# Optimization experiments

Measured on AMD Instinct MI355X. Metric: run time of the kernel, lower is better.

Reference implementation:

```python
import jax, jax.numpy as jnp
import numpy as np

S, B, D, H = 2048, 4, 1024, 16
HD = D // H  # 64
NEG = -1e9


def _rope_cache(seq_len, dim, base=10000.0):
    inv_freq = 1.0 / (base ** (jnp.arange(0, dim, 2, dtype=jnp.float32) / dim))
    pos = jnp.arange(seq_len, dtype=jnp.float32)
    freqs = jnp.einsum('i,j->ij', pos, inv_freq)          # [S, dim/2]
    emb = jnp.concatenate([freqs, freqs], axis=-1)         # [S, dim]
    return jnp.cos(emb)[None, None], jnp.sin(emb)[None, None]  # [1,1,S,dim]


def _apply_rotary(x, cos, sin):
    # rotated[..., ::2] = -x[..., 1::2]; rotated[..., 1::2] = x[..., ::2]
    x_even = x[..., ::2]
    x_odd = x[..., 1::2]
    rotated = jnp.stack([-x_odd, x_even], axis=-1).reshape(x.shape)
    return x * cos + rotated * sin


def setup_inputs() -> dict:
    key = jax.random.key(0)
    kx, kq, ko = jax.random.split(key, 3)
    x = jax.random.normal(kx, (S, B, D), dtype=jnp.float32)
    # additive causal mask, broadcastable over [B,H,S,S]
    causal = jnp.triu(jnp.full((S, S), NEG, dtype=jnp.float32), k=1)
    cos, sin = _rope_cache(S, HD)
    Wqkv = jax.random.normal(kq, (D, 3 * D), dtype=jnp.float32) * (D ** -0.5)
    Wout = jax.random.normal(ko, (D, D), dtype=jnp.float32) * (D ** -0.5)
    return {"x": x, "attn_mask": causal, "cos": cos, "sin": sin,
            "Wqkv": Wqkv, "Wout": Wout}


def reference(x, attn_mask, cos, sin, Wqkv, Wout):
    scale = 1.0 / jnp.sqrt(jnp.float32(HD))
    xb = jnp.swapaxes(x, 0, 1)                       # [B,S,D]
    qkv = jnp.einsum('bsd,de->bse', xb, Wqkv)        # [B,S,3D]
    q, k, v = jnp.split(qkv, 3, axis=-1)
    def heads(t):
        return t.reshape(B, S, H, HD).transpose(0, 2, 1, 3)  # [B,H,S,HD]
    q, k, v = heads(q), heads(k), heads(v)
    q = _apply_rotary(q, cos, sin)
    k = _apply_rotary(k, cos, sin)
    scores = jnp.einsum('bhsd,bhtd->bhst', q, k) * scale + attn_mask
    probs = jax.nn.softmax(scores, axis=-1)
    ctx = jnp.einsum('bhst,bhtd->bhsd', probs, v)
    ctx = ctx.transpose(0, 2, 1, 3).reshape(B, S, D)  # [B,S,D]
    out = jnp.einsum('bsd,de->bse', ctx, Wout)
    return jnp.swapaxes(out, 0, 1)                    # [S,B,D]
```

## Files before the change

kernel.cpp:

```cpp
#include <hip/hip_runtime.h>
#include <hip/hip_bf16.h>

#define S_LEN 2048
#define BATCH 4
#define DMODEL 1024
#define NHEAD 16
#define HDIM 64
#define E3 3072

typedef __bf16 bf16x8 __attribute__((ext_vector_type(8)));
typedef float f32x4 __attribute__((ext_vector_type(4)));

typedef const __attribute__((address_space(1))) void gvoid;
typedef __attribute__((address_space(3))) void lvoid;

__global__ void cast_f32_bf16(const float* __restrict__ src, __bf16* __restrict__ dst) {
    int i = (blockIdx.x * 256 + threadIdx.x) * 8;
    float4 a = *(const float4*)(src + i);
    float4 b = *(const float4*)(src + i + 4);
    bf16x8 v;
    v[0] = (__bf16)a.x; v[1] = (__bf16)a.y; v[2] = (__bf16)a.z; v[3] = (__bf16)a.w;
    v[4] = (__bf16)b.x; v[5] = (__bf16)b.y; v[6] = (__bf16)b.z; v[7] = (__bf16)b.w;
    *(bf16x8*)(dst + i) = v;
}

__global__ void transpose_f32_bf16(const float* __restrict__ src, __bf16* __restrict__ dst,
                                   int R, int C) {
    __shared__ float tile[32][33];
    int c0 = blockIdx.x * 32, r0 = blockIdx.y * 32;
    int tx = threadIdx.x, ty = threadIdx.y;
#pragma unroll
    for (int i = 0; i < 32; i += 8)
        tile[ty + i][tx] = src[(size_t)(r0 + ty + i) * C + c0 + tx];
    __syncthreads();
#pragma unroll
    for (int i = 0; i < 32; i += 8)
        dst[(size_t)(c0 + ty + i) * R + r0 + tx] = (__bf16)tile[tx][ty + i];
}

__global__ void transpose_v(const __bf16* __restrict__ qkv, __bf16* __restrict__ vt) {
    __shared__ unsigned short tile[64][65];
    int bh = blockIdx.y;
    int s0 = blockIdx.x * 64;
    int tx = threadIdx.x & 31, ty = threadIdx.x >> 5;
    const __bf16* src = qkv + (size_t)(bh >> 4) * S_LEN * E3 + 2 * DMODEL + (bh & 15) * HDIM;
#pragma unroll
    for (int i = 0; i < 8; i++) {
        ushort2 v = *(const ushort2*)(src + (size_t)(s0 + ty + i * 8) * E3 + 2 * tx);
        tile[2 * tx][ty + i * 8] = v.x;
        tile[2 * tx + 1][ty + i * 8] = v.y;
    }
    __syncthreads();
    __bf16* dst = vt + (size_t)bh * HDIM * S_LEN + s0;
#pragma unroll
    for (int i = 0; i < 8; i++) {
        ushort2 v;
        v.x = tile[ty + i * 8][2 * tx];
        v.y = tile[ty + i * 8][2 * tx + 1];
        *(ushort2*)(dst + (size_t)(ty + i * 8) * S_LEN + 2 * tx) = v;
    }
}

__global__ __launch_bounds__(256) void gemm_bt(
    const __bf16* __restrict__ A, const __bf16* __restrict__ BT, void* __restrict__ C,
    int K, int aSB, int aSS, int cSB, int cSS, int cF32) {
    __shared__ __bf16 lA[128 * 32];
    __shared__ __bf16 lB[128 * 32];

    const int tid = threadIdx.x;
    const int lane = tid & 63;
    const int quad = lane >> 4, l16 = lane & 15;
    const int wave = tid >> 6;
    const int wm = wave >> 1, wn = wave & 1;
    const int rm0 = blockIdx.y * 128;
    const int n0 = blockIdx.x * 128;
    const int bb = rm0 / S_LEN;
    const int s0 = rm0 % S_LEN;

    const int lrow = lane >> 2;
    const int lch = (lane & 3) * 8;
    const int row0 = wave * 32;
    const __bf16* gA0 = A + (size_t)bb * aSB + (size_t)(s0 + row0 + lrow) * aSS + lch;
    const __bf16* gA1 = A + (size_t)bb * aSB + (size_t)(s0 + row0 + 16 + lrow) * aSS + lch;
    const __bf16* gB0 = BT + (size_t)(n0 + row0 + lrow) * K + lch;
    const __bf16* gB1 = BT + (size_t)(n0 + row0 + 16 + lrow) * K + lch;
    __bf16* ldsA0 = &lA[row0 * 32];
    __bf16* ldsA1 = &lA[(row0 + 16) * 32];
    __bf16* ldsB0 = &lB[row0 * 32];
    __bf16* ldsB1 = &lB[(row0 + 16) * 32];

    f32x4 acc[4][4];
#pragma unroll
    for (int i = 0; i < 4; i++)
#pragma unroll
        for (int j = 0; j < 4; j++) acc[i][j] = (f32x4){0.f, 0.f, 0.f, 0.f};

    for (int k0 = 0; k0 < K; k0 += 32) {
        __builtin_amdgcn_global_load_lds((gvoid*)(gA0 + k0), (lvoid*)ldsA0, 16, 0, 0);
        __builtin_amdgcn_global_load_lds((gvoid*)(gA1 + k0), (lvoid*)ldsA1, 16, 0, 0);
        __builtin_amdgcn_global_load_lds((gvoid*)(gB0 + k0), (lvoid*)ldsB0, 16, 0, 0);
        __builtin_amdgcn_global_load_lds((gvoid*)(gB1 + k0), (lvoid*)ldsB1, 16, 0, 0);
        __syncthreads();

        bf16x8 aF[4], bF[4];
#pragma unroll
        for (int i = 0; i < 4; i++) {
            aF[i] = *(const bf16x8*)&lA[(wm * 64 + i * 16 + l16) * 32 + quad * 8];
            bF[i] = *(const bf16x8*)&lB[(wn * 64 + i * 16 + l16) * 32 + quad * 8];
        }
#pragma unroll
        for (int i = 0; i < 4; i++)
#pragma unroll
            for (int j = 0; j < 4; j++)
                acc[i][j] = __builtin_amdgcn_mfma_f32_16x16x32_bf16(aF[i], bF[j], acc[i][j], 0, 0, 0);
        __syncthreads();
    }

#pragma unroll
    for (int i = 0; i < 4; i++) {
        const int rl = wm * 64 + i * 16 + quad * 4;
#pragma unroll
        for (int r = 0; r < 4; r++) {
            const size_t rowOff = (size_t)bb * cSB + (size_t)(s0 + rl + r) * cSS + n0 + wn * 64 + l16;
            if (cF32) {
                float* cRow = (float*)C + rowOff;
#pragma unroll
                for (int j = 0; j < 4; j++) cRow[j * 16] = acc[i][j][r];
            } else {
                __bf16* cRow = (__bf16*)C + rowOff;
#pragma unroll
                for (int j = 0; j < 4; j++) cRow[j * 16] = (__bf16)acc[i][j][r];
            }
        }
    }
}

__global__ void rope_kernel(__bf16* __restrict__ qkv, const float* __restrict__ cosb,
                            const float* __restrict__ sinb) {
    int idx = blockIdx.x * 256 + threadIdx.x;
    int p2 = (idx & 31) * 2;
    int h = (idx >> 5) & 15;
    int part = (idx >> 9) & 1;
    int row = idx >> 10;
    int s = row & (S_LEN - 1);
    size_t base = (size_t)row * E3 + part * DMODEL + h * HDIM + p2;
    float x0 = (float)qkv[base];
    float x1 = (float)qkv[base + 1];
    float c0 = cosb[s * HDIM + p2];
    float c1 = cosb[s * HDIM + p2 + 1];
    float sn0 = sinb[s * HDIM + p2];
    float sn1 = sinb[s * HDIM + p2 + 1];
    qkv[base] = (__bf16)(x0 * c0 - x1 * sn0);
    qkv[base + 1] = (__bf16)(x1 * c1 + x0 * sn1);
}

#define VT_IDX(hd, t) ((hd) * 72 + ((hd) >> 4) * 8 + (t))

__global__ __launch_bounds__(256) void attn_kernel(const __bf16* __restrict__ qkv,
                                                   const __bf16* __restrict__ vt,
                                                   __bf16* __restrict__ ctx) {
    __shared__ __bf16 sK[64 * 72];
    __shared__ __bf16 sVT[64 * 72 + 32];
    __shared__ __bf16 sP[4 * 2 * 16 * 72];

    const int tid = threadIdx.x, lane = tid & 63, wave = tid >> 6;
    const int quad = lane >> 4, l16 = lane & 15;
    const int b = blockIdx.y >> 4, h = blockIdx.y & 15;
    const int pair = blockIdx.x;
    const int qtA = pair, qtB = 31 - pair;
    const int s0A = qtA * 64 + wave * 16;
    const int s0B = qtB * 64 + wave * 16;
    __bf16* PwA = &sP[wave * 2 * 16 * 72];
    __bf16* PwB = PwA + 16 * 72;

    const int srow = tid >> 2;
    const int c0 = (tid & 3) * 16;

    const float qscale = 0.125f * 1.44269504f;
    const __bf16* kBase = qkv + (size_t)(b * S_LEN + srow) * E3 + DMODEL + h * HDIM + c0;
    const __bf16* vBase = vt + ((size_t)blockIdx.y * HDIM + srow) * S_LEN + c0;

    const __bf16* qbA = qkv + (size_t)(b * S_LEN + s0A) * E3 + h * HDIM + (size_t)l16 * E3;
    const __bf16* qbB = qkv + (size_t)(b * S_LEN + s0B) * E3 + h * HDIM + (size_t)l16 * E3;
    bf16x8 qfA0 = *(const bf16x8*)(qbA + quad * 8);
    bf16x8 qfA1 = *(const bf16x8*)(qbA + 32 + quad * 8);
    bf16x8 qfB0 = *(const bf16x8*)(qbB + quad * 8);
    bf16x8 qfB1 = *(const bf16x8*)(qbB + 32 + quad * 8);
#pragma unroll
    for (int i = 0; i < 8; i++) {
        qfA0[i] = (__bf16)((float)qfA0[i] * qscale);
        qfA1[i] = (__bf16)((float)qfA1[i] * qscale);
        qfB0[i] = (__bf16)((float)qfB0[i] * qscale);
        qfB1[i] = (__bf16)((float)qfB1[i] * qscale);
    }

    f32x4 oA[4], oB[4], lacA, lacB;
#pragma unroll
    for (int j = 0; j < 4; j++) {
        oA[j] = (f32x4){0.f, 0.f, 0.f, 0.f};
        oB[j] = (f32x4){0.f, 0.f, 0.f, 0.f};
    }
    lacA = (f32x4){0.f, 0.f, 0.f, 0.f};
    lacB = (f32x4){0.f, 0.f, 0.f, 0.f};

    bf16x8 ones;
#pragma unroll
    for (int i = 0; i < 8; i++) ones[i] = (__bf16)1.0f;

    const __bf16* kRow = kBase;
    const __bf16* vRow = vBase;
    bf16x8 k0 = *(const bf16x8*)kRow;
    bf16x8 k1 = *(const bf16x8*)(kRow + 8);
    bf16x8 v0 = *(const bf16x8*)vRow;
    bf16x8 v1 = *(const bf16x8*)(vRow + 8);

    const int nT = qtB + 1;
#pragma unroll 1
    for (int it = 0; it < nT; ++it) {
        const int t0 = it * 64;
        *(bf16x8*)&sK[srow * 72 + c0] = k0;
        *(bf16x8*)&sK[srow * 72 + c0 + 8] = k1;
        *(bf16x8*)&sVT[VT_IDX(srow, c0)] = v0;
        *(bf16x8*)&sVT[VT_IDX(srow, c0 + 8)] = v1;
        __syncthreads();

        if (it + 1 < nT) {
            kRow += (size_t)64 * E3;
            vRow += 64;
            k0 = *(const bf16x8*)kRow;
            k1 = *(const bf16x8*)(kRow + 8);
            v0 = *(const bf16x8*)vRow;
            v1 = *(const bf16x8*)(vRow + 8);
        }

        const bool aAct = (it <= qtA);

        f32x4 scA[4], scB[4];
        __builtin_amdgcn_s_setprio(1);
#pragma unroll
        for (int j = 0; j < 4; j++) {
            bf16x8 kf0 = *(const bf16x8*)&sK[(j * 16 + l16) * 72 + quad * 8];
            bf16x8 kf1 = *(const bf16x8*)&sK[(j * 16 + l16) * 72 + 32 + quad * 8];
            f32x4 z = (f32x4){0.f, 0.f, 0.f, 0.f};
            z = __builtin_amdgcn_mfma_f32_16x16x32_bf16(qfB0, kf0, z, 0, 0, 0);
            scB[j] = __builtin_amdgcn_mfma_f32_16x16x32_bf16(qfB1, kf1, z, 0, 0, 0);
            if (aAct) {
                f32x4 za = (f32x4){0.f, 0.f, 0.f, 0.f};
                za = __builtin_amdgcn_mfma_f32_16x16x32_bf16(qfA0, kf0, za, 0, 0, 0);
                scA[j] = __builtin_amdgcn_mfma_f32_16x16x32_bf16(qfA1, kf1, za, 0, 0, 0);
            }
        }
        __builtin_amdgcn_s_setprio(0);

        if (it == qtB) {
#pragma unroll
            for (int j = 0; j < 4; j++)
#pragma unroll
                for (int r = 0; r < 4; r++) {
                    int sq = s0B + quad * 4 + r, st = t0 + j * 16 + l16;
                    float val = (st > sq) ? -1e9f : scB[j][r];
                    PwB[(quad * 4 + r) * 72 + j * 16 + l16] = (__bf16)__builtin_exp2f(val);
                }
        } else {
#pragma unroll
            for (int j = 0; j < 4; j++)
#pragma unroll
                for (int r = 0; r < 4; r++)
                    PwB[(quad * 4 + r) * 72 + j * 16 + l16] = (__bf16)__builtin_exp2f(scB[j][r]);
        }
        if (aAct) {
            if (it == qtA) {
#pragma unroll
                for (int j = 0; j < 4; j++)
#pragma unroll
                    for (int r = 0; r < 4; r++) {
                        int sq = s0A + quad * 4 + r, st = t0 + j * 16 + l16;
                        float val = (st > sq) ? -1e9f : scA[j][r];
                        PwA[(quad * 4 + r) * 72 + j * 16 + l16] = (__bf16)__builtin_exp2f(val);
                    }
            } else {
#pragma unroll
                for (int j = 0; j < 4; j++)
#pragma unroll
                    for (int r = 0; r < 4; r++)
                        PwA[(quad * 4 + r) * 72 + j * 16 + l16] = (__bf16)__builtin_exp2f(scA[j][r]);
            }
        }

        __builtin_amdgcn_s_setprio(1);
#pragma unroll
        for (int kt = 0; kt < 2; kt++) {
            bf16x8 pfB = *(const bf16x8*)&PwB[l16 * 72 + kt * 32 + quad * 8];
            bf16x8 pfA = pfB;
            if (aAct) pfA = *(const bf16x8*)&PwA[l16 * 72 + kt * 32 + quad * 8];
#pragma unroll
            for (int j = 0; j < 4; j++) {
                bf16x8 vf = *(const bf16x8*)&sVT[VT_IDX(j * 16 + l16, kt * 32 + quad * 8)];
                oB[j] = __builtin_amdgcn_mfma_f32_16x16x32_bf16(pfB, vf, oB[j], 0, 0, 0);
                if (aAct) oA[j] = __builtin_amdgcn_mfma_f32_16x16x32_bf16(pfA, vf, oA[j], 0, 0, 0);
            }
            lacB = __builtin_amdgcn_mfma_f32_16x16x32_bf16(pfB, ones, lacB, 0, 0, 0);
            if (aAct) lacA = __builtin_amdgcn_mfma_f32_16x16x32_bf16(pfA, ones, lacA, 0, 0, 0);
        }
        __builtin_amdgcn_s_setprio(0);
        __syncthreads();
    }

#pragma unroll
    for (int r = 0; r < 4; r++) {
        float inv = 1.f / lacA[r];
        size_t crow = (size_t)(b * S_LEN + s0A + quad * 4 + r) * DMODEL + h * HDIM + l16;
#pragma unroll
        for (int j = 0; j < 4; j++) ctx[crow + j * 16] = (__bf16)(oA[j][r] * inv);
    }
#pragma unroll
    for (int r = 0; r < 4; r++) {
        float inv = 1.f / lacB[r];
        size_t crow = (size_t)(b * S_LEN + s0B + quad * 4 + r) * DMODEL + h * HDIM + l16;
#pragma unroll
        for (int j = 0; j < 4; j++) ctx[crow + j * 16] = (__bf16)(oB[j][r] * inv);
    }
}

extern "C" void kernel_launch(void* const* d_in, const int* in_sizes, int n_in,
                              void* d_out, int out_size, void* d_ws, size_t ws_size,
                              hipStream_t stream) {
    const float* x = (const float*)d_in[0];
    const float* cosb = (const float*)d_in[2];
    const float* sinb = (const float*)d_in[3];
    const float* Wqkv = (const float*)d_in[4];
    const float* Wout = (const float*)d_in[5];
    float* out = (float*)d_out;

    char* ws = (char*)d_ws;
    __bf16* qkv = (__bf16*)ws;
    __bf16* ctx = (__bf16*)(ws + 50331648);
    __bf16* WqkvT = (__bf16*)(ws + 50331648 + 16777216);
    __bf16* WoutT = (__bf16*)(ws + 50331648 + 16777216 + 6291456);
    __bf16* xb = ctx;
    __bf16* vtg = (__bf16*)d_out;

    cast_f32_bf16<<<(S_LEN * BATCH * DMODEL / 8) / 256, 256, 0, stream>>>(x, xb);
    transpose_f32_bf16<<<dim3(E3 / 32, DMODEL / 32), dim3(32, 8), 0, stream>>>(Wqkv, WqkvT, DMODEL, E3);
    transpose_f32_bf16<<<dim3(DMODEL / 32, DMODEL / 32), dim3(32, 8), 0, stream>>>(Wout, WoutT, DMODEL, DMODEL);

    gemm_bt<<<dim3(E3 / 128, (BATCH * S_LEN) / 128), 256, 0, stream>>>(
        xb, WqkvT, qkv, DMODEL,
        DMODEL, BATCH * DMODEL,
        S_LEN * E3, E3, 0);

    transpose_v<<<dim3(S_LEN / 64, BATCH * NHEAD), 256, 0, stream>>>(qkv, vtg);

    rope_kernel<<<(BATCH * S_LEN * 2 * DMODEL / 2) / 256, 256, 0, stream>>>(qkv, cosb, sinb);

    attn_kernel<<<dim3(16, BATCH * NHEAD), 256, 0, stream>>>(qkv, vtg, ctx);

    gemm_bt<<<dim3(DMODEL / 128, (BATCH * S_LEN) / 128), 256, 0, stream>>>(
        ctx, WoutT, out, DMODEL,
        S_LEN * DMODEL, DMODEL,
        DMODEL, BATCH * DMODEL, 1);
}
```

Baseline: 349.3 us.

## Double-buffer attention K/V LDS, remap workgroups across XCDs, vectorize RoPE

The attention kernel now double-buffers the K and V^T LDS tiles and drops the trailing barrier, so each iteration needs one __syncthreads instead of two. Both the GEMM and the attention kernel remap block IDs so that neighbouring logical tiles land on the same XCD, which should improve L2 reuse. The RoPE kernel handles 8 bf16 elements per thread with vector loads and stores in place of scalar pairs. The cost is doubled K/V LDS in attention, which may lower occupancy. Removing the barrier also relies on the P buffers being per-wave and safe to reuse without it.

```diff
diff --git a/kernel.cpp b/kernel.cpp
--- a/kernel.cpp
+++ b/kernel.cpp
@@ -72,8 +72,15 @@
     const int quad = lane >> 4, l16 = lane & 15;
     const int wave = tid >> 6;
     const int wm = wave >> 1, wn = wave & 1;
-    const int rm0 = blockIdx.y * 128;
-    const int n0 = blockIdx.x * 128;
+
+    const int bid0 = blockIdx.y * gridDim.x + blockIdx.x;
+    const int nwg = gridDim.x * gridDim.y;
+    const int lid = (bid0 & 7) * (nwg >> 3) + (bid0 >> 3);
+    const int bx = lid % gridDim.x;
+    const int by = lid / gridDim.x;
+
+    const int rm0 = by * 128;
+    const int n0 = bx * 128;
     const int bb = rm0 / S_LEN;
     const int s0 = rm0 % S_LEN;
 
@@ -138,20 +145,34 @@
 __global__ void rope_kernel(__bf16* __restrict__ qkv, const float* __restrict__ cosb,
                             const float* __restrict__ sinb) {
     int idx = blockIdx.x * 256 + threadIdx.x;
-    int p2 = (idx & 31) * 2;
-    int h = (idx >> 5) & 15;
-    int part = (idx >> 9) & 1;
-    int row = idx >> 10;
+    int t8 = idx & 7;
+    int h = (idx >> 3) & 15;
+    int part = (idx >> 7) & 1;
+    int row = idx >> 8;
     int s = row & (S_LEN - 1);
-    size_t base = (size_t)row * E3 + part * DMODEL + h * HDIM + p2;
-    float x0 = (float)qkv[base];
-    float x1 = (float)qkv[base + 1];
-    float c0 = cosb[s * HDIM + p2];
-    float c1 = cosb[s * HDIM + p2 + 1];
-    float sn0 = sinb[s * HDIM + p2];
-    float sn1 = sinb[s * HDIM + p2 + 1];
-    qkv[base] = (__bf16)(x0 * c0 - x1 * sn0);
-    qkv[base + 1] = (__bf16)(x1 * c1 + x0 * sn1);
+    size_t base = (size_t)row * E3 + part * DMODEL + h * HDIM + t8 * 8;
+    bf16x8 v = *(const bf16x8*)(qkv + base);
+    const float* cp = cosb + s * HDIM + t8 * 8;
+    const float* sp = sinb + s * HDIM + t8 * 8;
+    float4 c0 = *(const float4*)cp;
+    float4 c1 = *(const float4*)(cp + 4);
+    float4 s0 = *(const float4*)sp;
+    float4 s1 = *(const float4*)(sp + 4);
+    bf16x8 o;
+    float x0, x1;
+    x0 = (float)v[0]; x1 = (float)v[1];
+    o[0] = (__bf16)(x0 * c0.x - x1 * s0.x);
+    o[1] = (__bf16)(x1 * c0.y + x0 * s0.y);
+    x0 = (float)v[2]; x1 = (float)v[3];
+    o[2] = (__bf16)(x0 * c0.z - x1 * s0.z);
+    o[3] = (__bf16)(x1 * c0.w + x0 * s0.w);
+    x0 = (float)v[4]; x1 = (float)v[5];
+    o[4] = (__bf16)(x0 * c1.x - x1 * s1.x);
+    o[5] = (__bf16)(x1 * c1.y + x0 * s1.y);
+    x0 = (float)v[6]; x1 = (float)v[7];
+    o[6] = (__bf16)(x0 * c1.z - x1 * s1.z);
+    o[7] = (__bf16)(x1 * c1.w + x0 * s1.w);
+    *(bf16x8*)(qkv + base) = o;
 }
 
 #define VT_IDX(hd, t) ((hd) * 72 + ((hd) >> 4) * 8 + (t))
@@ -159,14 +180,19 @@
 __global__ __launch_bounds__(256) void attn_kernel(const __bf16* __restrict__ qkv,
                                                    const __bf16* __restrict__ vt,
                                                    __bf16* __restrict__ ctx) {
-    __shared__ __bf16 sK[64 * 72];
-    __shared__ __bf16 sVT[64 * 72 + 32];
+    __shared__ __bf16 sK[2][64 * 72];
+    __shared__ __bf16 sVT[2][64 * 72 + 32];
     __shared__ __bf16 sP[4 * 2 * 16 * 72];
 
     const int tid = threadIdx.x, lane = tid & 63, wave = tid >> 6;
     const int quad = lane >> 4, l16 = lane & 15;
-    const int b = blockIdx.y >> 4, h = blockIdx.y & 15;
-    const int pair = blockIdx.x;
+
+    const int bid0 = blockIdx.y * 16 + blockIdx.x;
+    const int lid = (bid0 & 7) * 128 + (bid0 >> 3);
+    const int pair = lid & 15;
+    const int bh = lid >> 4;
+    const int b = bh >> 4, h = bh & 15;
+
     const int qtA = pair, qtB = 31 - pair;
     const int s0A = qtA * 64 + wave * 16;
     const int s0B = qtB * 64 + wave * 16;
@@ -178,7 +204,7 @@
 
     const float qscale = 0.125f * 1.44269504f;
     const __bf16* kBase = qkv + (size_t)(b * S_LEN + srow) * E3 + DMODEL + h * HDIM + c0;
-    const __bf16* vBase = vt + ((size_t)blockIdx.y * HDIM + srow) * S_LEN + c0;
+    const __bf16* vBase = vt + ((size_t)bh * HDIM + srow) * S_LEN + c0;
 
     const __bf16* qbA = qkv + (size_t)(b * S_LEN + s0A) * E3 + h * HDIM + (size_t)l16 * E3;
     const __bf16* qbB = qkv + (size_t)(b * S_LEN + s0B) * E3 + h * HDIM + (size_t)l16 * E3;
@@ -218,10 +244,12 @@
 #pragma unroll 1
     for (int it = 0; it < nT; ++it) {
         const int t0 = it * 64;
-        *(bf16x8*)&sK[srow * 72 + c0] = k0;
-        *(bf16x8*)&sK[srow * 72 + c0 + 8] = k1;
-        *(bf16x8*)&sVT[VT_IDX(srow, c0)] = v0;
-        *(bf16x8*)&sVT[VT_IDX(srow, c0 + 8)] = v1;
+        __bf16* sKc = sK[it & 1];
+        __bf16* sVc = sVT[it & 1];
+        *(bf16x8*)&sKc[srow * 72 + c0] = k0;
+        *(bf16x8*)&sKc[srow * 72 + c0 + 8] = k1;
+        *(bf16x8*)&sVc[VT_IDX(srow, c0)] = v0;
+        *(bf16x8*)&sVc[VT_IDX(srow, c0 + 8)] = v1;
         __syncthreads();
 
         if (it + 1 < nT) {
@@ -239,8 +267,8 @@
         __builtin_amdgcn_s_setprio(1);
 #pragma unroll
         for (int j = 0; j < 4; j++) {
-            bf16x8 kf0 = *(const bf16x8*)&sK[(j * 16 + l16) * 72 + quad * 8];
-            bf16x8 kf1 = *(const bf16x8*)&sK[(j * 16 + l16) * 72 + 32 + quad * 8];
+            bf16x8 kf0 = *(const bf16x8*)&sKc[(j * 16 + l16) * 72 + quad * 8];
+            bf16x8 kf1 = *(const bf16x8*)&sKc[(j * 16 + l16) * 72 + 32 + quad * 8];
             f32x4 z = (f32x4){0.f, 0.f, 0.f, 0.f};
             z = __builtin_amdgcn_mfma_f32_16x16x32_bf16(qfB0, kf0, z, 0, 0, 0);
             scB[j] = __builtin_amdgcn_mfma_f32_16x16x32_bf16(qfB1, kf1, z, 0, 0, 0);
@@ -295,7 +323,7 @@
             if (aAct) pfA = *(const bf16x8*)&PwA[l16 * 72 + kt * 32 + quad * 8];
 #pragma unroll
             for (int j = 0; j < 4; j++) {
-                bf16x8 vf = *(const bf16x8*)&sVT[VT_IDX(j * 16 + l16, kt * 32 + quad * 8)];
+                bf16x8 vf = *(const bf16x8*)&sVc[VT_IDX(j * 16 + l16, kt * 32 + quad * 8)];
                 oB[j] = __builtin_amdgcn_mfma_f32_16x16x32_bf16(pfB, vf, oB[j], 0, 0, 0);
                 if (aAct) oA[j] = __builtin_amdgcn_mfma_f32_16x16x32_bf16(pfA, vf, oA[j], 0, 0, 0);
             }
@@ -303,7 +331,6 @@
             if (aAct) lacA = __builtin_amdgcn_mfma_f32_16x16x32_bf16(pfA, ones, lacA, 0, 0, 0);
         }
         __builtin_amdgcn_s_setprio(0);
-        __syncthreads();
     }
 
 #pragma unroll
@@ -351,7 +378,7 @@
 
     transpose_v<<<dim3(S_LEN / 64, BATCH * NHEAD), 256, 0, stream>>>(qkv, vtg);
 
-    rope_kernel<<<(BATCH * S_LEN * 2 * DMODEL / 2) / 256, 256, 0, stream>>>(qkv, cosb, sinb);
+    rope_kernel<<<(BATCH * S_LEN * 2 * DMODEL / 8) / 256, 256, 0, stream>>>(qkv, cosb, sinb);
 
     attn_kernel<<<dim3(16, BATCH * NHEAD), 256, 0, stream>>>(qkv, vtg, ctx);
 
```

Result: faster. 337.6 us (-3.3%).
